# Kernel optimization log

Hardware: AMD Instinct MI355X
Metric: run time of the kernel (lower is better)

The kernel has to match this reference:

```python
import jax, jax.numpy as jnp
import numpy as np

RES = 0.03
NUM_ROTS = 36
NUM_PROPOSAL = 256
OVERSAMPLE = 4           # fixed-size stand-in for the data-dependent while loop
GX, GY, GZ = 272, 112, 272  # grid covering [-4,4.16] x [-0.2,3.16] x [-4,4.16] at res=0.03
POW = 0.5
SEED_DIST_THRESH = 0.3


def setup_inputs() -> dict:
    key = jax.random.key(0)
    ks = jax.random.split(key, 6)
    N, M = 100000, 1024
    extent = jnp.array([7.0, 3.0, 7.0], jnp.float32)
    offset = jnp.array([-3.5, 0.0, -3.5], jnp.float32)
    pc = jax.random.uniform(ks[0], (N, 3), jnp.float32) * extent + offset
    xyz = jax.random.uniform(ks[1], (N, 3), jnp.float32, minval=-0.3, maxval=0.3)
    scale = jax.random.uniform(ks[2], (N, 3), jnp.float32, minval=0.1, maxval=1.0)
    prob = jax.random.uniform(ks[3], (N,), jnp.float32)
    corners = jnp.array([[-4.0, -0.2, -4.0], [4.16, 3.16, 4.16]], jnp.float32)
    vote_points = jax.random.uniform(ks[4], (M, 3), jnp.float32) * extent + offset
    return dict(pc=pc, xyz=xyz, scale=scale, prob=prob, corners=corners, vote_points=vote_points)


def hough_vote(pc, xyz, scale, prob, corners):
    # Each point casts NUM_ROTS votes: center = pc + R_y(theta) @ xyz_offset
    thetas = 2.0 * jnp.pi * jnp.arange(NUM_ROTS, dtype=jnp.float32) / NUM_ROTS
    c, s = jnp.cos(thetas), jnp.sin(thetas)  # [R]
    ox, oy, oz = xyz[:, 0:1], xyz[:, 1:2], xyz[:, 2:3]  # [N,1]
    rx = ox * c + oz * s      # [N,R]
    rz = -ox * s + oz * c     # [N,R]
    tx = pc[:, 0:1] + rx
    ty = jnp.broadcast_to(pc[:, 1:2] + oy, tx.shape)
    tz = pc[:, 2:3] + rz
    ix = jnp.floor((tx - corners[0, 0]) / RES + 0.5).astype(jnp.int32)
    iy = jnp.floor((ty - corners[0, 1]) / RES + 0.5).astype(jnp.int32)
    iz = jnp.floor((tz - corners[0, 2]) / RES + 0.5).astype(jnp.int32)
    inb = ((ix >= 0) & (ix < GX) & (iy >= 0) & (iy < GY) & (iz >= 0) & (iz < GZ))
    ixc = jnp.clip(ix, 0, GX - 1)
    iyc = jnp.clip(iy, 0, GY - 1)
    izc = jnp.clip(iz, 0, GZ - 1)
    flat = ((ixc * GY + iyc) * GZ + izc).ravel()  # [N*R]
    w = (prob[:, None] * inb.astype(prob.dtype))  # [N,R]
    grid_obj = jnp.zeros((GX * GY * GZ,), pc.dtype).at[flat].add(w.ravel())
    ws = (w[:, :, None] * scale[:, None, :]).reshape(-1, 3)
    grid_scale = jnp.zeros((GX * GY * GZ, 3), pc.dtype).at[flat].add(ws)
    hv_map = grid_obj.reshape(GX, GY, GZ)
    hv_scale = (grid_scale / (grid_obj[:, None] + 1e-7)).reshape(GX, GY, GZ, 3)
    return hv_map, hv_scale


def reference(pc, xyz, scale, prob, corners, vote_points):
    hv_map, hv_scale = hough_vote(pc, xyz, scale, prob, corners)
    hv_map_y = jnp.power(hv_map.max(axis=1) + 1e-7, POW)  # [GX,GZ]
    hv_map_yidx = jnp.argmax(hv_map, axis=1)              # [GX,GZ]
    dist = hv_map_y.reshape(-1)
    finite = jnp.isfinite(dist)
    safe = jnp.where(finite, dist, 0.0)
    ok = finite.all() & (safe.sum() >= 1e-7)
    dist = jnp.where(ok, safe, 1.0)

    # fixed-size oversampling instead of the data-dependent while loop
    K = NUM_PROPOSAL * OVERSAMPLE
    sample = jax.random.categorical(jax.random.key(42), jnp.log(dist + 1e-30), shape=(K,))
    sample_val = dist[sample]
    xi = sample // GZ
    zi = sample % GZ
    yi = hv_map_yidx[xi, zi]
    world_loc = jnp.stack([xi, yi, zi], -1).astype(pc.dtype) * RES + corners[0]  # [K,3]
    sc = hv_scale[xi, yi, zi, :]  # [K,3]

    # min distance to vote seeds; keep candidates near seeds (fallback: keep all)
    d2seed = jnp.min(jnp.linalg.norm(world_loc[:, None, :] - vote_points[None, :, :], axis=-1), axis=-1)
    keep = d2seed < SEED_DIST_THRESH
    keep = jnp.where(keep.any(), keep, jnp.ones_like(keep))
    order = jnp.argsort(jnp.where(keep, 0, 1))  # stable: passing candidates first
    sel = order[:NUM_PROPOSAL]
    candidates = world_loc[sel]
    scales_out = sc[sel]
    probs = jnp.zeros((NUM_PROPOSAL,), pc.dtype)
    return candidates, probs, scales_out
```

## Files before the change

kernel.cpp:

```cpp
#include <hip/hip_runtime.h>
#include <math.h>
#include <stdio.h>
#include <stdint.h>

#define GXD 272
#define GYD 112
#define GZD 272
#define NROT 36
#define CCLS (GXD*GZD)
#define KSMP 1024
#define NPROP 256
#define HSLOTS 2048
#define YH 56
#define NBINS (GXD*2)
#define SLICE (GYD*GZD)
#define SVCAP 64
#define ROWG 32

struct RotTab { float c[NROT]; float s[NROT]; };

__device__ __forceinline__ uint32_t cell_hash(int flat) {
    return ((uint32_t)flat * 2654435761u) >> 21;
}

#define ROTL_AB(x, r) __builtin_amdgcn_alignbit((x), (x), 32u - (r))

__device__ __forceinline__ uint32_t tf_bits(uint32_t i) {
    constexpr uint32_t K1  = 42u;
    constexpr uint32_t KS2 = 42u ^ 0x1BD11BDAu;
    uint32_t x0 = 0u, x1 = i + K1;
#define TF_R(r)  { x0 += x1; x1 = ROTL_AB(x1, r); x1 ^= x0; }
#define TF_RI(r, I0, I1) { x1 += (I1); x0 = x0 + (I0) + x1; x1 = ROTL_AB(x1, r); x1 ^= x0; }
    TF_R(13) TF_R(15) TF_R(26) TF_R(6)
    TF_RI(17, K1,  KS2 + 1u)  TF_R(29) TF_R(16) TF_R(24)
    TF_RI(13, KS2, 2u)        TF_R(15) TF_R(26) TF_R(6)
    TF_RI(17, 0u,  K1 + 3u)   TF_R(29) TF_R(16) TF_R(24)
    TF_RI(13, K1,  KS2 + 4u)  TF_R(15) TF_R(26) TF_R(6)
#undef TF_R
#undef TF_RI
    return (x0 + KS2) ^ (x1 + 5u);
}

__device__ __forceinline__ float uniform_from_bits(uint32_t b) {
    const float TINY = 1.1754943508222875e-38f;
    float f = __uint_as_float((b >> 9) | 0x3f800000u) - 1.0f;
    float u = __fadd_rn(__fmul_rn(f, 1.0f), TINY);
    return fmaxf(TINY, u);
}

__device__ __forceinline__ float gumbel_from_u(float u) {
    float l1 = (float)log((double)u);
    float l2 = (float)log((double)(-l1));
    return -l2;
}

__device__ __forceinline__ bool vote_iy(float py, float oy, float c0y, int& iy) {
    float ty = __fadd_rn(py, oy);
    float vy = __fadd_rn(__fdiv_rn(__fsub_rn(ty, c0y), 0.03f), 0.5f);
    iy = (int)floorf(vy);
    return (iy >= 0 && iy < GYD);
}
__device__ __forceinline__ bool vote_xz(float px, float pz, float ox, float oz,
                                        float c, float s, float c0x, float c0z,
                                        int& ix, int& iz) {
    float rx = __fadd_rn(__fmul_rn(ox, c), __fmul_rn(oz, s));
    float rz = __fadd_rn(__fmul_rn(-ox, s), __fmul_rn(oz, c));
    float tx = __fadd_rn(px, rx);
    float tz = __fadd_rn(pz, rz);
    float vx = __fadd_rn(__fdiv_rn(__fsub_rn(tx, c0x), 0.03f), 0.5f);
    float vz = __fadd_rn(__fdiv_rn(__fsub_rn(tz, c0z), 0.03f), 0.5f);
    ix = (int)floorf(vx);
    iz = (int)floorf(vz);
    return (ix >= 0 && ix < GXD && iz >= 0 && iz < GZD);
}

__global__ __launch_bounds__(256) void k_count(const float* __restrict__ pc, const float* __restrict__ xyz,
                          const float* __restrict__ corners, int N, RotTab rt,
                          int* __restrict__ bincnt) {
    __shared__ int h[NBINS];
    int tid = threadIdx.x;
    for (int j = tid; j < NBINS; j += 256) h[j] = 0;
    __syncthreads();
    int i = blockIdx.x * 256 + tid;
    if (i < N) {
        float px = pc[3*i], py = pc[3*i+1], pz = pc[3*i+2];
        float ox = xyz[3*i], oy = xyz[3*i+1], oz = xyz[3*i+2];
        int iy;
        if (vote_iy(py, oy, corners[1], iy)) {
            int ybit = (iy >= YH) ? 1 : 0;
            float c0x = corners[0], c0z = corners[2];
            for (int r = 0; r < NROT; ++r) {
                int ix, iz;
                if (vote_xz(px, pz, ox, oz, rt.c[r], rt.s[r], c0x, c0z, ix, iz))
                    atomicAdd(&h[ix*2 + ybit], 1);
            }
        }
    }
    __syncthreads();
    for (int j = tid; j < NBINS; j += 256) if (h[j]) atomicAdd(&bincnt[j], h[j]);
}

__global__ __launch_bounds__(576) void k_prefix(const int* __restrict__ bincnt,
                         int* __restrict__ binbase, int* __restrict__ bincur) {
    __shared__ int sc[576];
    int tid = threadIdx.x;
    int v = (tid < NBINS) ? bincnt[tid] : 0;
    sc[tid] = v;
    __syncthreads();
    for (int off = 1; off < 576; off <<= 1) {
        int x = sc[tid];
        if (tid >= off) x += sc[tid - off];
        __syncthreads();
        sc[tid] = x;
        __syncthreads();
    }
    if (tid < NBINS) {
        int excl = sc[tid] - v;
        binbase[tid] = excl;
        bincur[tid] = excl;
    }
}

__global__ __launch_bounds__(256) void k_binwrite(const float* __restrict__ pc, const float* __restrict__ xyz,
                          const float* __restrict__ prob, const float* __restrict__ corners,
                          int N, RotTab rt, int* __restrict__ bincur,
                          uint2* __restrict__ vrec) {
    __shared__ int h[NBINS];
    __shared__ int bbase[NBINS];
    int tid = threadIdx.x;
    for (int j = tid; j < NBINS; j += 256) h[j] = 0;
    __syncthreads();
    int i = blockIdx.x * 256 + tid;
    float px=0, py=0, pz=0, ox=0, oy=0, oz=0, w0=0, c0x=0, c0z=0;
    int iy = -1, ybit = 0;
    bool act = false;
    if (i < N) {
        px = pc[3*i]; py = pc[3*i+1]; pz = pc[3*i+2];
        ox = xyz[3*i]; oy = xyz[3*i+1]; oz = xyz[3*i+2];
        w0 = prob[i];
        c0x = corners[0]; c0z = corners[2];
        if (vote_iy(py, oy, corners[1], iy)) {
            act = true;
            ybit = (iy >= YH) ? 1 : 0;
        }
    }
    if (act) {
        for (int r = 0; r < NROT; ++r) {
            int ix, iz;
            if (vote_xz(px, pz, ox, oz, rt.c[r], rt.s[r], c0x, c0z, ix, iz))
                atomicAdd(&h[ix*2 + ybit], 1);
        }
    }
    __syncthreads();
    for (int j = tid; j < NBINS; j += 256) {
        int cnt = h[j];
        bbase[j] = cnt ? atomicAdd(&bincur[j], cnt) : 0;
        h[j] = 0;
    }
    __syncthreads();
    if (act) {
        for (int r = 0; r < NROT; ++r) {
            int ix, iz;
            if (vote_xz(px, pz, ox, oz, rt.c[r], rt.s[r], c0x, c0z, ix, iz)) {
                int bin = ix*2 + ybit;
                int rank = atomicAdd(&h[bin], 1);
                int slot = bbase[bin] + rank;
                vrec[slot] = make_uint2((uint32_t)((ix*GYD + iy)*GZD + iz), __float_as_uint(w0));
            }
        }
    }
}

__global__ __launch_bounds__(256) void k_accum(const int* __restrict__ binbase,
                          const int* __restrict__ bincnt,
                          const uint2* __restrict__ vrec,
                          float* __restrict__ gobj,
                          float* __restrict__ cmax, int* __restrict__ camax) {
    __shared__ float tile[YH*GZD];
    int b = blockIdx.x;
    int x = b >> 1, yh = b & 1;
    int tid = threadIdx.x;
    for (int j = tid; j < YH*GZD; j += 256) tile[j] = 0.0f;
    __syncthreads();
    int lo = binbase[b], n = bincnt[b];
    int xoff = x * SLICE;
    int yoff = yh * (YH*GZD);
    int sub = xoff + yoff;
    for (int j = lo + tid; j < lo + n; j += 256) {
        uint2 rec = vrec[j];
        atomicAdd(&tile[(int)rec.x - sub], __uint_as_float(rec.y));
    }
    __syncthreads();
    float* dst = gobj + (size_t)sub;
    for (int j = tid; j < YH*GZD; j += 256) dst[j] = tile[j];
    for (int z = tid; z < GZD; z += 256) {
        float m = tile[z];
        int mi = 0;
        for (int y = 1; y < YH; ++y) {
            float v = tile[y*GZD + z];
            if (v > m) { m = v; mi = y; }
        }
        cmax[b*GZD + z] = m;
        camax[b*GZD + z] = mi;
    }
}

__global__ __launch_bounds__(256) void k_colmax2(const float* __restrict__ cmax,
                         const int* __restrict__ camax,
                         float* __restrict__ logits, int* __restrict__ yidx,
                         float* __restrict__ sumdist) {
    int c = blockIdx.x * blockDim.x + threadIdx.x;
    float d = 0.0f;
    if (c < CCLS) {
        int x = c / GZD, z = c % GZD;
        int b0 = (x*2)*GZD + z;
        int b1 = b0 + GZD;
        float m0 = cmax[b0], m1 = cmax[b1];
        float m; int mi;
        if (m1 > m0) { m = m1; mi = YH + camax[b1]; }
        else         { m = m0; mi = camax[b0]; }
        d = __fsqrt_rn(__fadd_rn(m, 1e-7f));
        yidx[c] = mi;
        logits[c] = (float)log((double)__fadd_rn(d, 1e-30f));
    }
    __shared__ float sred[256];
    int tid = threadIdx.x;
    sred[tid] = d; __syncthreads();
    for (int off = 128; off > 0; off >>= 1) {
        if (tid < off) sred[tid] += sred[tid+off];
        __syncthreads();
    }
    if (tid == 0) atomicAdd(sumdist, sred[0]);
}

__global__ __launch_bounds__(256) void k_thresh(const float* __restrict__ logits,
                                                const float* __restrict__ sumdist,
                                                uint32_t* __restrict__ bth) {
    int c = blockIdx.x * blockDim.x + threadIdx.x;
    if (c >= CCLS) return;
    double B0 = log((double)*sumdist) - 3.0;
    double t = exp(-exp((double)logits[c] - (B0 - 0.05)));
    long long k_th = (long long)floor(t * 8388608.0) - 2;
    uint32_t b;
    if (k_th <= 0)              b = 0u;
    else if (k_th >= 8388608LL) b = 0xFFFFFFFFu;
    else                        b = (uint32_t)k_th << 9;
    bth[c] = b;
}

__global__ __launch_bounds__(256) void k_prefilter(const uint32_t* __restrict__ bth,
                                                   int* __restrict__ svcnt,
                                                   uint2* __restrict__ svrec) {
    int c = blockIdx.x * 256 + threadIdx.x;
    int k0 = blockIdx.y * (KSMP / ROWG);
    uint32_t th = bth[c];
    uint32_t i = (uint32_t)k0 * (uint32_t)CCLS + (uint32_t)c;
#pragma unroll 4
    for (int kk = 0; kk < KSMP / ROWG; ++kk) {
        uint32_t bits = tf_bits(i);
        if (__builtin_expect(bits >= th, 0)) {
            int row = k0 + kk;
            int idx = atomicAdd(&svcnt[row], 1);
            if (idx < SVCAP) svrec[row * SVCAP + idx] = make_uint2((uint32_t)c, bits);
        }
        i += (uint32_t)CCLS;
    }
}

__global__ __launch_bounds__(64) void k_finalize(const float* __restrict__ logits,
                                                 const int* __restrict__ svcnt,
                                                 const uint2* __restrict__ svrec,
                                                 int* __restrict__ samples) {
    int k = blockIdx.x;
    int tid = threadIdx.x;
    int n = svcnt[k];
    float best = -INFINITY; int bc = 0x7fffffff;
    if (n > 0 && n <= SVCAP) {
        if (tid < n) {
            uint2 rec = svrec[k * SVCAP + tid];
            int c = (int)rec.x;
            best = __fadd_rn(gumbel_from_u(uniform_from_bits(rec.y)), logits[c]);
            bc = c;
        }
    } else {
        uint32_t base = (uint32_t)k * (uint32_t)CCLS;
        for (int c = tid; c < CCLS; c += 64) {
            float v = __fadd_rn(gumbel_from_u(uniform_from_bits(tf_bits(base + (uint32_t)c))), logits[c]);
            if (v > best || (v == best && c < bc)) { best = v; bc = c; }
        }
    }
    for (int off = 32; off > 0; off >>= 1) {
        float v2 = __shfl_down(best, off);
        int   i2 = __shfl_down(bc, off);
        if (v2 > best || (v2 == best && i2 < bc)) { best = v2; bc = i2; }
    }
    if (tid == 0) samples[k] = bc;
}

__global__ __launch_bounds__(256) void k_build_table(const int* __restrict__ samples,
                                                     const int* __restrict__ yidx,
                                                     int* __restrict__ hkeys,
                                                     float* __restrict__ gsmall) {
    int tid = threadIdx.x;
    for (int j = tid; j < HSLOTS; j += 256) hkeys[j] = -1;
    for (int j = tid; j < 3*HSLOTS; j += 256) gsmall[j] = 0.0f;
    __syncthreads();
    for (int k = tid; k < KSMP; k += 256) {
        int s = samples[k];
        int xi = s / GZD, zi = s % GZD;
        int yi = yidx[s];
        int flat = (xi*GYD + yi)*GZD + zi;
        uint32_t h = cell_hash(flat);
        for (;;) {
            int prev = atomicCAS(&hkeys[h], -1, flat);
            if (prev == -1 || prev == flat) break;
            h = (h + 1) & (HSLOTS - 1);
        }
    }
}

__global__ __launch_bounds__(256) void k_scale_scatter(const float* __restrict__ pc, const float* __restrict__ xyz,
                          const float* __restrict__ scale, const float* __restrict__ prob,
                          const float* __restrict__ corners,
                          const int* __restrict__ hkeys, float* __restrict__ gsmall,
                          int N, RotTab rt) {
    __shared__ int lk[HSLOTS];
    for (int j = threadIdx.x; j < HSLOTS; j += 256) lk[j] = hkeys[j];
    __syncthreads();
    int i = blockIdx.x * 256 + threadIdx.x;
    if (i >= N) return;
    float px = pc[3*i], py = pc[3*i+1], pz = pc[3*i+2];
    float ox = xyz[3*i], oy = xyz[3*i+1], oz = xyz[3*i+2];
    int iy;
    if (!vote_iy(py, oy, corners[1], iy)) return;
    float c0x = corners[0], c0z = corners[2];
    int iyo = iy * GZD;
    float w0 = prob[i];
    float ws0 = __fmul_rn(w0, scale[3*i]);
    float ws1 = __fmul_rn(w0, scale[3*i+1]);
    float ws2 = __fmul_rn(w0, scale[3*i+2]);
    for (int r = 0; r < NROT; ++r) {
        int ix, iz;
        if (!vote_xz(px, pz, ox, oz, rt.c[r], rt.s[r], c0x, c0z, ix, iz)) continue;
        int flat = ix * SLICE + iyo + iz;
        uint32_t h = cell_hash(flat);
        int slot = -1;
        for (;;) {
            int key = lk[h];
            if (key == flat) { slot = (int)h; break; }
            if (key == -1) break;
            h = (h + 1) & (HSLOTS - 1);
        }
        if (slot < 0) continue;
        atomicAdd(&gsmall[3*slot+0], ws0);
        atomicAdd(&gsmall[3*slot+1], ws1);
        atomicAdd(&gsmall[3*slot+2], ws2);
    }
}

__global__ __launch_bounds__(256) void k_post(const float* __restrict__ gobj,
                       const int* __restrict__ hkeys, const float* __restrict__ gsmall,
                       const int* __restrict__ yidx, const int* __restrict__ samples,
                       const float* __restrict__ corners, const float* __restrict__ vp, int M,
                       float* __restrict__ world, float* __restrict__ scv, int* __restrict__ keep) {
    int k = blockIdx.x;
    int tid = threadIdx.x;
    int s = samples[k];
    int xi = s / GZD, zi = s % GZD;
    int yi = yidx[s];
    float wx = __fadd_rn(__fmul_rn((float)xi, 0.03f), corners[0]);
    float wy = __fadd_rn(__fmul_rn((float)yi, 0.03f), corners[1]);
    float wz = __fadd_rn(__fmul_rn((float)zi, 0.03f), corners[2]);

    float dmin = INFINITY;
    for (int j = tid; j < M; j += 256) {
        float dx = __fsub_rn(wx, vp[3*j]);
        float dy = __fsub_rn(wy, vp[3*j+1]);
        float dz = __fsub_rn(wz, vp[3*j+2]);
        float sq = __fadd_rn(__fadd_rn(__fmul_rn(dx,dx), __fmul_rn(dy,dy)), __fmul_rn(dz,dz));
        dmin = fminf(dmin, __fsqrt_rn(sq));
    }
    __shared__ float sm[256];
    sm[tid] = dmin; __syncthreads();
    for (int off = 128; off > 0; off >>= 1) {
        if (tid < off) sm[tid] = fminf(sm[tid], sm[tid+off]);
        __syncthreads();
    }
    if (tid == 0) {
        world[3*k] = wx; world[3*k+1] = wy; world[3*k+2] = wz;
        int flat = (xi*GYD + yi)*GZD + zi;
        uint32_t h = cell_hash(flat);
        while (hkeys[h] != flat) h = (h + 1) & (HSLOTS - 1);
        float go = __fadd_rn(gobj[flat], 1e-7f);
        scv[3*k+0] = __fdiv_rn(gsmall[3*h+0], go);
        scv[3*k+1] = __fdiv_rn(gsmall[3*h+1], go);
        scv[3*k+2] = __fdiv_rn(gsmall[3*h+2], go);
        keep[k] = (sm[0] < 0.3f) ? 1 : 0;
    }
}

__global__ __launch_bounds__(256) void k_select(const float* __restrict__ world,
                                                const float* __restrict__ scv,
                                                const int* __restrict__ keep,
                                                float* __restrict__ out) {
    __shared__ int kp[KSMP];
    __shared__ int tsum[256];
    __shared__ int sel[NPROP];
    __shared__ int anyk;
    int tid = threadIdx.x;
    if (tid == 0) anyk = 0;
    __syncthreads();
    int a = 0;
    for (int j = tid; j < KSMP; j += 256) { int v = keep[j]; kp[j] = v; a |= v; }
    if (a) anyk = 1;
    __syncthreads();
    int any = anyk;
    int j0 = tid * 4;
    int k0v = any ? kp[j0]   : 1;
    int k1v = any ? kp[j0+1] : 1;
    int k2v = any ? kp[j0+2] : 1;
    int k3v = any ? kp[j0+3] : 1;
    int s0 = k0v, s1 = s0 + k1v, s2 = s1 + k2v, s3 = s2 + k3v;
    tsum[tid] = s3;
    __syncthreads();
    for (int off = 1; off < 256; off <<= 1) {
        int x = tsum[tid];
        if (tid >= off) x += tsum[tid - off];
        __syncthreads();
        tsum[tid] = x;
        __syncthreads();
    }
    int base = (tid > 0) ? tsum[tid-1] : 0;
    int nk = tsum[255];
    int inc[4] = { base + s0, base + s1, base + s2, base + s3 };
    int kv[4]  = { k0v, k1v, k2v, k3v };
    for (int q = 0; q < 4; ++q) {
        int j = j0 + q;
        int slot = kv[q] ? (inc[q] - 1) : (nk + j - inc[q]);
        if (slot < NPROP) sel[slot] = j;
    }
    __syncthreads();
    if (tid < NPROP) {
        int sidx = sel[tid];
        out[3*tid+0] = world[3*sidx+0];
        out[3*tid+1] = world[3*sidx+1];
        out[3*tid+2] = world[3*sidx+2];
        out[3*NPROP + tid] = 0.0f;
        out[4*NPROP + 3*tid + 0] = scv[3*sidx+0];
        out[4*NPROP + 3*tid + 1] = scv[3*sidx+1];
        out[4*NPROP + 3*tid + 2] = scv[3*sidx+2];
    }
}

extern "C" void kernel_launch(void* const* d_in, const int* in_sizes, int n_in,
                              void* d_out, int out_size, void* d_ws, size_t ws_size,
                              hipStream_t stream) {
    const float* pc      = (const float*)d_in[0];
    const float* xyz     = (const float*)d_in[1];
    const float* scale   = (const float*)d_in[2];
    const float* prob    = (const float*)d_in[3];
    const float* corners = (const float*)d_in[4];
    const float* vp      = (const float*)d_in[5];
    int N = in_sizes[0] / 3;
    int M = in_sizes[5] / 3;
    int NV = N * NROT;

    const size_t G = (size_t)GXD * GYD * GZD;
    float* gobj    = (float*)d_ws;
    float* sumdist = gobj + G;
    int*   bincnt  = (int*)(sumdist + 1);
    int*   svcnt   = bincnt + NBINS;
    int*   binbase = svcnt + KSMP;
    int*   bincur  = binbase + NBINS;
    float* logits  = (float*)(bincur + NBINS);
    uint32_t* bth  = (uint32_t*)(logits + CCLS);
    int*   yidx    = (int*)(bth + CCLS);
    int*   samples = yidx + CCLS;
    int*   hkeys   = samples + KSMP;
    float* gsmall  = (float*)(hkeys + HSLOTS);
    float* world   = gsmall + 3*HSLOTS;
    float* scv     = world + 3*KSMP;
    int*   keep    = (int*)(scv + 3*KSMP);
    float* cmax    = (float*)(keep + KSMP);
    int*   camax   = (int*)(cmax + (size_t)NBINS*GZD);
    uint2* svrec   = (uint2*)(((uintptr_t)(camax + (size_t)NBINS*GZD) + 15) & ~(uintptr_t)15);
    uint2* vrec    = svrec + (size_t)KSMP * SVCAP;
    size_t need = (size_t)((char*)(vrec + NV) - (char*)d_ws);
    if (ws_size < need) {
        fprintf(stderr, "kernel_launch: ws_size %zu < needed %zu\n", ws_size, need);
        return;
    }

    hipMemsetAsync(sumdist, 0, (1 + NBINS + KSMP)*sizeof(int), stream);

    RotTab rt;
    const float twopi = (float)(2.0 * M_PI);
    for (int r = 0; r < NROT; ++r) {
        float th = (twopi * (float)r) / 36.0f;
        rt.c[r] = (float)cos((double)th);
        rt.s[r] = (float)sin((double)th);
    }

    int pblocks = (N + 255) / 256;
    k_count<<<pblocks, 256, 0, stream>>>(pc, xyz, corners, N, rt, bincnt);
    k_prefix<<<1, 576, 0, stream>>>(bincnt, binbase, bincur);
    k_binwrite<<<pblocks, 256, 0, stream>>>(pc, xyz, prob, corners, N, rt, bincur, vrec);
    k_accum<<<NBINS, 256, 0, stream>>>(binbase, bincnt, vrec, gobj, cmax, camax);
    k_colmax2<<<CCLS / 256, 256, 0, stream>>>(cmax, camax, logits, yidx, sumdist);
    k_thresh<<<CCLS / 256, 256, 0, stream>>>(logits, sumdist, bth);
    dim3 pf_grid(CCLS / 256, ROWG);
    k_prefilter<<<pf_grid, 256, 0, stream>>>(bth, svcnt, svrec);
    k_finalize<<<KSMP, 64, 0, stream>>>(logits, svcnt, svrec, samples);
    k_build_table<<<1, 256, 0, stream>>>(samples, yidx, hkeys, gsmall);
    k_scale_scatter<<<pblocks, 256, 0, stream>>>(pc, xyz, scale, prob, corners, hkeys, gsmall, N, rt);
    k_post<<<KSMP, 256, 0, stream>>>(gobj, hkeys, gsmall, yidx, samples, corners, vp, M, world, scv, keep);
    k_select<<<1, 256, 0, stream>>>(world, scv, keep, (float*)d_out);
}
```

Before: 400.2 us.

## Reuse per-block histograms, pack column argmax atomically, fold table build into finalize

k_count now saves each block's bin histogram to workspace, so k_binwrite no longer recomputes the 36-rotation counting pass before claiming slots. k_accum publishes the per-half column max and y index through a 64-bit atomicMax on a packed key, which removes the cmax/camax arrays and lets k_colmax2 read a single value. The separate single-block k_build_table kernel is removed; its hash insertion moves into k_finalize's thread 0, and the table initialisation becomes memsets. In exchange it adds per-block histogram writes and reads plus global 64-bit atomics, and relies on the packed key ordering (value, then lower y index) to keep the original tie-breaking.

Result: no change. 393.5 us (-1.7%).

```diff
diff --git a/kernel.cpp b/kernel.cpp
--- a/kernel.cpp
+++ b/kernel.cpp
@@ -76,7 +76,7 @@
 
 __global__ __launch_bounds__(256) void k_count(const float* __restrict__ pc, const float* __restrict__ xyz,
                           const float* __restrict__ corners, int N, RotTab rt,
-                          int* __restrict__ bincnt) {
+                          int* __restrict__ bincnt, int* __restrict__ hblk) {
     __shared__ int h[NBINS];
     int tid = threadIdx.x;
     for (int j = tid; j < NBINS; j += 256) h[j] = 0;
@@ -97,7 +97,12 @@
         }
     }
     __syncthreads();
-    for (int j = tid; j < NBINS; j += 256) if (h[j]) atomicAdd(&bincnt[j], h[j]);
+    int* hb = hblk + (size_t)blockIdx.x * NBINS;
+    for (int j = tid; j < NBINS; j += 256) {
+        int cnt = h[j];
+        hb[j] = cnt;
+        if (cnt) atomicAdd(&bincnt[j], cnt);
+    }
 }
 
 __global__ __launch_bounds__(576) void k_prefix(const int* __restrict__ bincnt,
@@ -124,48 +129,34 @@
 __global__ __launch_bounds__(256) void k_binwrite(const float* __restrict__ pc, const float* __restrict__ xyz,
                           const float* __restrict__ prob, const float* __restrict__ corners,
                           int N, RotTab rt, int* __restrict__ bincur,
-                          uint2* __restrict__ vrec) {
+                          const int* __restrict__ hblk, uint2* __restrict__ vrec) {
     __shared__ int h[NBINS];
     __shared__ int bbase[NBINS];
     int tid = threadIdx.x;
-    for (int j = tid; j < NBINS; j += 256) h[j] = 0;
-    __syncthreads();
-    int i = blockIdx.x * 256 + tid;
-    float px=0, py=0, pz=0, ox=0, oy=0, oz=0, w0=0, c0x=0, c0z=0;
-    int iy = -1, ybit = 0;
-    bool act = false;
-    if (i < N) {
-        px = pc[3*i]; py = pc[3*i+1]; pz = pc[3*i+2];
-        ox = xyz[3*i]; oy = xyz[3*i+1]; oz = xyz[3*i+2];
-        w0 = prob[i];
-        c0x = corners[0]; c0z = corners[2];
-        if (vote_iy(py, oy, corners[1], iy)) {
-            act = true;
-            ybit = (iy >= YH) ? 1 : 0;
-        }
-    }
-    if (act) {
-        for (int r = 0; r < NROT; ++r) {
-            int ix, iz;
-            if (vote_xz(px, pz, ox, oz, rt.c[r], rt.s[r], c0x, c0z, ix, iz))
-                atomicAdd(&h[ix*2 + ybit], 1);
-        }
-    }
-    __syncthreads();
+    const int* hb = hblk + (size_t)blockIdx.x * NBINS;
     for (int j = tid; j < NBINS; j += 256) {
-        int cnt = h[j];
+        int cnt = hb[j];
         bbase[j] = cnt ? atomicAdd(&bincur[j], cnt) : 0;
         h[j] = 0;
     }
     __syncthreads();
-    if (act) {
-        for (int r = 0; r < NROT; ++r) {
-            int ix, iz;
-            if (vote_xz(px, pz, ox, oz, rt.c[r], rt.s[r], c0x, c0z, ix, iz)) {
-                int bin = ix*2 + ybit;
-                int rank = atomicAdd(&h[bin], 1);
-                int slot = bbase[bin] + rank;
-                vrec[slot] = make_uint2((uint32_t)((ix*GYD + iy)*GZD + iz), __float_as_uint(w0));
+    int i = blockIdx.x * 256 + tid;
+    if (i < N) {
+        float px = pc[3*i], py = pc[3*i+1], pz = pc[3*i+2];
+        float ox = xyz[3*i], oy = xyz[3*i+1], oz = xyz[3*i+2];
+        int iy;
+        if (vote_iy(py, oy, corners[1], iy)) {
+            int ybit = (iy >= YH) ? 1 : 0;
+            float c0x = corners[0], c0z = corners[2];
+            float w0 = prob[i];
+            for (int r = 0; r < NROT; ++r) {
+                int ix, iz;
+                if (vote_xz(px, pz, ox, oz, rt.c[r], rt.s[r], c0x, c0z, ix, iz)) {
+                    int bin = ix*2 + ybit;
+                    int rank = atomicAdd(&h[bin], 1);
+                    int slot = bbase[bin] + rank;
+                    vrec[slot] = make_uint2((uint32_t)((ix*GYD + iy)*GZD + iz), __float_as_uint(w0));
+                }
             }
         }
     }
@@ -175,7 +166,7 @@
                           const int* __restrict__ bincnt,
                           const uint2* __restrict__ vrec,
                           float* __restrict__ gobj,
-                          float* __restrict__ cmax, int* __restrict__ camax) {
+                          unsigned long long* __restrict__ packed) {
     __shared__ float tile[YH*GZD];
     int b = blockIdx.x;
     int x = b >> 1, yh = b & 1;
@@ -193,6 +184,7 @@
     __syncthreads();
     float* dst = gobj + (size_t)sub;
     for (int j = tid; j < YH*GZD; j += 256) dst[j] = tile[j];
+    int ybase = yh * YH;
     for (int z = tid; z < GZD; z += 256) {
         float m = tile[z];
         int mi = 0;
@@ -200,29 +192,22 @@
             float v = tile[y*GZD + z];
             if (v > m) { m = v; mi = y; }
         }
-        cmax[b*GZD + z] = m;
-        camax[b*GZD + z] = mi;
-    }
-}
-
-__global__ __launch_bounds__(256) void k_colmax2(const float* __restrict__ cmax,
-                         const int* __restrict__ camax,
+        unsigned long long key = ((unsigned long long)__float_as_uint(m) << 32)
+                               | (unsigned long long)(uint32_t)(0x7F - (ybase + mi));
+        atomicMax(&packed[x*GZD + z], key);
+    }
+}
+
+__global__ __launch_bounds__(256) void k_colmax2(const unsigned long long* __restrict__ packed,
                          float* __restrict__ logits, int* __restrict__ yidx,
                          float* __restrict__ sumdist) {
     int c = blockIdx.x * blockDim.x + threadIdx.x;
-    float d = 0.0f;
-    if (c < CCLS) {
-        int x = c / GZD, z = c % GZD;
-        int b0 = (x*2)*GZD + z;
-        int b1 = b0 + GZD;
-        float m0 = cmax[b0], m1 = cmax[b1];
-        float m; int mi;
-        if (m1 > m0) { m = m1; mi = YH + camax[b1]; }
-        else         { m = m0; mi = camax[b0]; }
-        d = __fsqrt_rn(__fadd_rn(m, 1e-7f));
-        yidx[c] = mi;
-        logits[c] = (float)log((double)__fadd_rn(d, 1e-30f));
-    }
+    unsigned long long key = packed[c];
+    float m = __uint_as_float((uint32_t)(key >> 32));
+    int mi = 0x7F - (int)(uint32_t)(key & 0xFFFFFFFFu);
+    float d = __fsqrt_rn(__fadd_rn(m, 1e-7f));
+    yidx[c] = mi;
+    logits[c] = (float)log((double)__fadd_rn(d, 1e-30f));
     __shared__ float sred[256];
     int tid = threadIdx.x;
     sred[tid] = d; __syncthreads();
@@ -270,6 +255,8 @@
 __global__ __launch_bounds__(64) void k_finalize(const float* __restrict__ logits,
                                                  const int* __restrict__ svcnt,
                                                  const uint2* __restrict__ svrec,
+                                                 const int* __restrict__ yidx,
+                                                 int* __restrict__ hkeys,
                                                  int* __restrict__ samples) {
     int k = blockIdx.x;
     int tid = threadIdx.x;
@@ -294,21 +281,10 @@
         int   i2 = __shfl_down(bc, off);
         if (v2 > best || (v2 == best && i2 < bc)) { best = v2; bc = i2; }
     }
-    if (tid == 0) samples[k] = bc;
-}
-
-__global__ __launch_bounds__(256) void k_build_table(const int* __restrict__ samples,
-                                                     const int* __restrict__ yidx,
-                                                     int* __restrict__ hkeys,
-                                                     float* __restrict__ gsmall) {
-    int tid = threadIdx.x;
-    for (int j = tid; j < HSLOTS; j += 256) hkeys[j] = -1;
-    for (int j = tid; j < 3*HSLOTS; j += 256) gsmall[j] = 0.0f;
-    __syncthreads();
-    for (int k = tid; k < KSMP; k += 256) {
-        int s = samples[k];
-        int xi = s / GZD, zi = s % GZD;
-        int yi = yidx[s];
+    if (tid == 0) {
+        samples[k] = bc;
+        int xi = bc / GZD, zi = bc % GZD;
+        int yi = yidx[bc];
         int flat = (xi*GYD + yi)*GZD + zi;
         uint32_t h = cell_hash(flat);
         for (;;) {
@@ -464,34 +440,37 @@
     int N = in_sizes[0] / 3;
     int M = in_sizes[5] / 3;
     int NV = N * NROT;
+    int pblocks = (N + 255) / 256;
 
     const size_t G = (size_t)GXD * GYD * GZD;
     float* gobj    = (float*)d_ws;
     float* sumdist = gobj + G;
     int*   bincnt  = (int*)(sumdist + 1);
     int*   svcnt   = bincnt + NBINS;
-    int*   binbase = svcnt + KSMP;
+    unsigned long long* packed = (unsigned long long*)(svcnt + KSMP + 1);
+    float* gsmall  = (float*)(packed + CCLS);
+    size_t zero_bytes = (size_t)((char*)(gsmall + 3*HSLOTS) - (char*)sumdist);
+    int*   binbase = (int*)(gsmall + 3*HSLOTS);
     int*   bincur  = binbase + NBINS;
     float* logits  = (float*)(bincur + NBINS);
     uint32_t* bth  = (uint32_t*)(logits + CCLS);
     int*   yidx    = (int*)(bth + CCLS);
     int*   samples = yidx + CCLS;
     int*   hkeys   = samples + KSMP;
-    float* gsmall  = (float*)(hkeys + HSLOTS);
-    float* world   = gsmall + 3*HSLOTS;
+    float* world   = (float*)(hkeys + HSLOTS);
     float* scv     = world + 3*KSMP;
     int*   keep    = (int*)(scv + 3*KSMP);
-    float* cmax    = (float*)(keep + KSMP);
-    int*   camax   = (int*)(cmax + (size_t)NBINS*GZD);
-    uint2* svrec   = (uint2*)(((uintptr_t)(camax + (size_t)NBINS*GZD) + 15) & ~(uintptr_t)15);
-    uint2* vrec    = svrec + (size_t)KSMP * SVCAP;
+    uint2* svrec   = (uint2*)(((uintptr_t)(keep + KSMP) + 15) & ~(uintptr_t)15);
+    int*   hblk    = (int*)(svrec + (size_t)KSMP * SVCAP);
+    uint2* vrec    = (uint2*)(((uintptr_t)(hblk + (size_t)pblocks*NBINS) + 15) & ~(uintptr_t)15);
     size_t need = (size_t)((char*)(vrec + NV) - (char*)d_ws);
     if (ws_size < need) {
         fprintf(stderr, "kernel_launch: ws_size %zu < needed %zu\n", ws_size, need);
         return;
     }
 
-    hipMemsetAsync(sumdist, 0, (1 + NBINS + KSMP)*sizeof(int), stream);
+    hipMemsetAsync(sumdist, 0, zero_bytes, stream);
+    hipMemsetAsync(hkeys, 0xFF, HSLOTS*sizeof(int), stream);
 
     RotTab rt;
     const float twopi = (float)(2.0 * M_PI);
@@ -501,17 +480,15 @@
         rt.s[r] = (float)sin((double)th);
     }
 
-    int pblocks = (N + 255) / 256;
-    k_count<<<pblocks, 256, 0, stream>>>(pc, xyz, corners, N, rt, bincnt);
+    k_count<<<pblocks, 256, 0, stream>>>(pc, xyz, corners, N, rt, bincnt, hblk);
     k_prefix<<<1, 576, 0, stream>>>(bincnt, binbase, bincur);
-    k_binwrite<<<pblocks, 256, 0, stream>>>(pc, xyz, prob, corners, N, rt, bincur, vrec);
-    k_accum<<<NBINS, 256, 0, stream>>>(binbase, bincnt, vrec, gobj, cmax, camax);
-    k_colmax2<<<CCLS / 256, 256, 0, stream>>>(cmax, camax, logits, yidx, sumdist);
+    k_binwrite<<<pblocks, 256, 0, stream>>>(pc, xyz, prob, corners, N, rt, bincur, hblk, vrec);
+    k_accum<<<NBINS, 256, 0, stream>>>(binbase, bincnt, vrec, gobj, packed);
+    k_colmax2<<<CCLS / 256, 256, 0, stream>>>(packed, logits, yidx, sumdist);
     k_thresh<<<CCLS / 256, 256, 0, stream>>>(logits, sumdist, bth);
     dim3 pf_grid(CCLS / 256, ROWG);
     k_prefilter<<<pf_grid, 256, 0, stream>>>(bth, svcnt, svrec);
-    k_finalize<<<KSMP, 64, 0, stream>>>(logits, svcnt, svrec, samples);
-    k_build_table<<<1, 256, 0, stream>>>(samples, yidx, hkeys, gsmall);
+    k_finalize<<<KSMP, 64, 0, stream>>>(logits, svcnt, svrec, yidx, hkeys, samples);
     k_scale_scatter<<<pblocks, 256, 0, stream>>>(pc, xyz, scale, prob, corners, hkeys, gsmall, N, rt);
     k_post<<<KSMP, 256, 0, stream>>>(gobj, hkeys, gsmall, yidx, samples, corners, vp, M, world, scv, keep);
     k_select<<<1, 256, 0, stream>>>(world, scv, keep, (float*)d_out);
```
